# Kernel tuning notes

Hardware: AMD Instinct MI355X
Metric: run time of the kernel (lower is better)

## Reference

```python
import jax, jax.numpy as jnp
import numpy as np

N_NODES = 100000
N_EDGES = 1000000
D = 128          # in_features
C = 86           # out_classes (DDI relation types)


def setup_inputs() -> dict:
    key = jax.random.key(0)
    k_h, k_src, k_dst, k_w1, k_b1, k_w2, k_b2 = jax.random.split(key, 7)
    h = jax.random.normal(k_h, (N_NODES, D), dtype=jnp.float32)
    src = jax.random.randint(k_src, (N_EDGES,), 0, N_NODES, dtype=jnp.int64)
    dst = jax.random.randint(k_dst, (N_EDGES,), 0, N_NODES, dtype=jnp.int64)
    # nn.Linear default init: U(-1/sqrt(fan_in), 1/sqrt(fan_in))
    lim1 = 1.0 / np.sqrt(2 * D)
    W1 = jax.random.uniform(k_w1, (2 * D, D), jnp.float32, -lim1, lim1)
    b1 = jax.random.uniform(k_b1, (D,), jnp.float32, -lim1, lim1)
    lim2 = 1.0 / np.sqrt(D)
    W2 = jax.random.uniform(k_w2, (D, C), jnp.float32, -lim2, lim2)
    b2 = jax.random.uniform(k_b2, (C,), jnp.float32, -lim2, lim2)
    return {"h": h, "W1": W1, "b1": b1, "W2": W2, "b2": b2,
            "src": src, "dst": dst}


def reference(h, W1, b1, W2, b2, src, dst):
    # Gather per-edge src/dst node features: [E, D] each
    h_u = h[src]
    h_v = h[dst]
    # Split W1 along its input dim instead of materializing concat [E, 2D]
    # (same math as cat([h_u, h_v], 1) @ W1)
    W1u, W1v = W1[:D], W1[D:]
    hid = jax.nn.relu(h_u @ W1u + h_v @ W1v + b1)   # [E, D]
    score = hid @ W2 + b2                            # [E, C]
    return score
```

## Files before the change

kernel.cpp:

```cpp
#include <hip/hip_runtime.h>


typedef short bf16x8 __attribute__((ext_vector_type(8)));
typedef float f32x4 __attribute__((ext_vector_type(4)));

#define DIM 128
#define C_OUT 86
#define NPAD 96
#define HSTRIDE 136

__device__ __forceinline__ float bf2f(unsigned short u) {
    unsigned int x = ((unsigned int)u) << 16;
    float f;
    __builtin_memcpy(&f, &x, 4);
    return f;
}
__device__ __forceinline__ unsigned short f2bf(float f) {
    unsigned int x;
    __builtin_memcpy(&x, &f, 4);
    x = x + 0x7fffu + ((x >> 16) & 1u);
    return (unsigned short)(x >> 16);
}

__global__ __launch_bounds__(256) void node_gemm_kernel(
    const float* __restrict__ h, const float* __restrict__ W1,
    unsigned short* __restrict__ PQ, int n_nodes)
{
    __shared__ float As[64][33];
    __shared__ float Bs[32][64];
    const int t = threadIdx.x;
    const int m0 = blockIdx.x * 64;
    const int n0 = blockIdx.y * 64;
    const float* Bbase = (n0 < 128) ? (W1 + n0) : (W1 + 128 * 128 + (n0 - 128));
    const int tx = t & 15, ty = t >> 4;
    float acc[4][4] = {};
    for (int k0 = 0; k0 < 128; k0 += 32) {
#pragma unroll
        for (int i = 0; i < 2; ++i) {
            int f = t + i * 256;
            int r = f >> 3;
            int kc = (f & 7) << 2;
            int gr = m0 + r;
            float4 v = make_float4(0.f, 0.f, 0.f, 0.f);
            if (gr < n_nodes) v = *(const float4*)(h + (size_t)gr * DIM + k0 + kc);
            As[r][kc + 0] = v.x; As[r][kc + 1] = v.y;
            As[r][kc + 2] = v.z; As[r][kc + 3] = v.w;
        }
#pragma unroll
        for (int i = 0; i < 2; ++i) {
            int f = t + i * 256;
            int kk = f >> 4;
            int jc = (f & 15) << 2;
            *(float4*)&Bs[kk][jc] = *(const float4*)(Bbase + (size_t)(k0 + kk) * DIM + jc);
        }
        __syncthreads();
#pragma unroll
        for (int kk = 0; kk < 32; ++kk) {
            float a[4], b[4];
#pragma unroll
            for (int r = 0; r < 4; ++r) a[r] = As[ty * 4 + r][kk];
#pragma unroll
            for (int c = 0; c < 4; ++c) b[c] = Bs[kk][tx * 4 + c];
#pragma unroll
            for (int r = 0; r < 4; ++r)
#pragma unroll
                for (int c = 0; c < 4; ++c) acc[r][c] += a[r] * b[c];
        }
        __syncthreads();
    }
#pragma unroll
    for (int r = 0; r < 4; ++r) {
        int gm = m0 + ty * 4 + r;
        if (gm < n_nodes) {
            ushort4 o = make_ushort4(f2bf(acc[r][0]), f2bf(acc[r][1]),
                                     f2bf(acc[r][2]), f2bf(acc[r][3]));
            *(ushort4*)(PQ + (size_t)gm * 256 + n0 + tx * 4) = o;
        }
    }
}

__global__ __launch_bounds__(256) void edge_mlp_kernel(
    const unsigned short* __restrict__ PQ,
    const float* __restrict__ b1,
    const float* __restrict__ W2,
    const float* __restrict__ b2,
    const int* __restrict__ src,
    const int* __restrict__ dst,
    float* __restrict__ out,
    int n_edges)
{
    __shared__ unsigned short W2T[NPAD * HSTRIDE];
    __shared__ unsigned short hidL[64 * HSTRIDE];
    __shared__ float b1s[DIM];
    __shared__ float b2s[NPAD];

    const int t = threadIdx.x;
    for (int i = t; i < NPAD * DIM; i += 256) {
        int n = i >> 7;
        int k = i & 127;
        float v = (n < C_OUT) ? W2[(size_t)k * C_OUT + n] : 0.f;
        W2T[n * HSTRIDE + k] = f2bf(v);
    }
    if (t < DIM) b1s[t] = b1[t];
    if (t < NPAD) b2s[t] = (t < C_OUT) ? b2[t] : 0.f;
    __syncthreads();

    const int lane = t & 63;
    const int wv = t >> 6;
    const int m = lane & 15;
    const int quad = lane >> 4;

    bf16x8 Bfrag[6][4];
#pragma unroll
    for (int nt = 0; nt < 6; ++nt)
#pragma unroll
        for (int kt = 0; kt < 4; ++kt)
            Bfrag[nt][kt] = *(const bf16x8*)&W2T[(nt * 16 + m) * HSTRIDE + kt * 32 + quad * 8];

    const ushort4* PQ4 = (const ushort4*)PQ;

    for (int e0 = blockIdx.x * 64; e0 < n_edges; e0 += gridDim.x * 64) {
#pragma unroll
        for (int i = 0; i < 8; ++i) {
            int qi = t + i * 256;
            int e = qi >> 5;
            int q = qi & 31;
            int edge = e0 + e;
            ushort4 hv = make_ushort4(0, 0, 0, 0);
            if (edge < n_edges) {
                int s = src[edge];
                int d = dst[edge];
                ushort4 pv = PQ4[(size_t)s * 64 + q];
                ushort4 qv = PQ4[(size_t)d * 64 + 32 + q];
                int k = q << 2;
                float4 bb = *(const float4*)&b1s[k];
                float x0 = fmaxf(bf2f(pv.x) + bf2f(qv.x) + bb.x, 0.f);
                float x1 = fmaxf(bf2f(pv.y) + bf2f(qv.y) + bb.y, 0.f);
                float x2 = fmaxf(bf2f(pv.z) + bf2f(qv.z) + bb.z, 0.f);
                float x3 = fmaxf(bf2f(pv.w) + bf2f(qv.w) + bb.w, 0.f);
                hv = make_ushort4(f2bf(x0), f2bf(x1), f2bf(x2), f2bf(x3));
            }
            *(ushort4*)&hidL[e * HSTRIDE + (q << 2)] = hv;
        }
        __syncthreads();

        bf16x8 af[4];
#pragma unroll
        for (int kt = 0; kt < 4; ++kt)
            af[kt] = *(const bf16x8*)&hidL[(wv * 16 + m) * HSTRIDE + kt * 32 + quad * 8];

#pragma unroll
        for (int nt = 0; nt < 6; ++nt) {
            f32x4 acc = {0.f, 0.f, 0.f, 0.f};
#pragma unroll
            for (int kt = 0; kt < 4; ++kt)
                acc = __builtin_amdgcn_mfma_f32_16x16x32_bf16(af[kt], Bfrag[nt][kt], acc, 0, 0, 0);
            int col = nt * 16 + m;
            if (col < C_OUT) {
                float bias = b2s[col];
                int ebase = e0 + wv * 16 + quad * 4;
#pragma unroll
                for (int r = 0; r < 4; ++r) {
                    int edge = ebase + r;
                    if (edge < n_edges)
                        out[(size_t)edge * C_OUT + col] = acc[r] + bias;
                }
            }
        }
        __syncthreads();
    }
}

extern "C" void kernel_launch(void* const* d_in, const int* in_sizes, int n_in,
                              void* d_out, int out_size, void* d_ws, size_t ws_size,
                              hipStream_t stream) {
    const float* h  = (const float*)d_in[0];
    const float* W1 = (const float*)d_in[1];
    const float* b1 = (const float*)d_in[2];
    const float* W2 = (const float*)d_in[3];
    const float* b2 = (const float*)d_in[4];
    const int* src  = (const int*)d_in[5];
    const int* dst  = (const int*)d_in[6];
    float* out = (float*)d_out;
    const int n_nodes = in_sizes[0] / DIM;
    const int n_edges = in_sizes[5];
    unsigned short* PQ = (unsigned short*)d_ws;

    node_gemm_kernel<<<dim3((n_nodes + 63) / 64, 4), 256, 0, stream>>>(h, W1, PQ, n_nodes);
    edge_mlp_kernel<<<dim3(768), 256, 0, stream>>>(PQ, b1, W2, b2, src, dst, out, n_edges);
}
```

Before: 620.7 us.

## Use MFMA with split-bf16 for node GEMM and gather edge rows directly into registers

The node GEMM moves from scalar fp32 FMAs to bf16 MFMA. Each h value is split into a high and a low bf16 part to keep accuracy close to fp32, W1 is pre-packed in LDS in fragment layout, and b1 is folded into the Q half. The edge kernel drops the shared-memory hidden staging and its barriers: each lane gathers its edge's P and Q rows as 16-byte vectors straight into MFMA A fragments. W2 fragments are read from LDS instead of being held in registers, and both kernels get persistent grids and occupancy hints. In exchange the node GEMM does twice the MFMA work and writes scalar bf16 stores, and bf16 rounding of PQ and the hidden values remains.

New measurement: 865.8 us. 39.5% more time.

```diff
diff --git a/kernel.cpp b/kernel.cpp
--- a/kernel.cpp
+++ b/kernel.cpp
@@ -7,7 +7,6 @@
 #define DIM 128
 #define C_OUT 86
 #define NPAD 96
-#define HSTRIDE 136
 
 __device__ __forceinline__ float bf2f(unsigned short u) {
     unsigned int x = ((unsigned int)u) << 16;
@@ -22,66 +21,75 @@
     return (unsigned short)(x >> 16);
 }
 
-__global__ __launch_bounds__(256) void node_gemm_kernel(
+__global__ __launch_bounds__(256, 5) void node_gemm_kernel(
     const float* __restrict__ h, const float* __restrict__ W1,
+    const float* __restrict__ b1,
     unsigned short* __restrict__ PQ, int n_nodes)
 {
-    __shared__ float As[64][33];
-    __shared__ float Bs[32][64];
+    __shared__ unsigned short W1p[8 * 4 * 64 * 8];
     const int t = threadIdx.x;
-    const int m0 = blockIdx.x * 64;
-    const int n0 = blockIdx.y * 64;
-    const float* Bbase = (n0 < 128) ? (W1 + n0) : (W1 + 128 * 128 + (n0 - 128));
-    const int tx = t & 15, ty = t >> 4;
-    float acc[4][4] = {};
-    for (int k0 = 0; k0 < 128; k0 += 32) {
+    const int half = blockIdx.y;
+
+    for (int i = t; i < 128 * 128; i += 256) {
+        int k = i >> 7;
+        int jn = i & 127;
+        float v = W1[(size_t)(half * 128 + k) * 128 + jn];
+        int nt = jn >> 4, m = jn & 15;
+        int kt = k >> 5, quad = (k >> 3) & 3, jj = k & 7;
+        W1p[(((nt * 4 + kt) * 64) + quad * 16 + m) * 8 + jj] = f2bf(v);
+    }
+    __syncthreads();
+
+    const int lane = t & 63;
+    const int wv = t >> 6;
+    const int m = lane & 15;
+    const int quad = lane >> 4;
+    const bf16x8* bp = (const bf16x8*)W1p;
+
+    float bias[8];
 #pragma unroll
-        for (int i = 0; i < 2; ++i) {
-            int f = t + i * 256;
-            int r = f >> 3;
-            int kc = (f & 7) << 2;
-            int gr = m0 + r;
-            float4 v = make_float4(0.f, 0.f, 0.f, 0.f);
-            if (gr < n_nodes) v = *(const float4*)(h + (size_t)gr * DIM + k0 + kc);
-            As[r][kc + 0] = v.x; As[r][kc + 1] = v.y;
-            As[r][kc + 2] = v.z; As[r][kc + 3] = v.w;
+    for (int nt = 0; nt < 8; ++nt) bias[nt] = half ? b1[nt * 16 + m] : 0.f;
+
+    for (int m0 = blockIdx.x * 64; m0 < n_nodes; m0 += gridDim.x * 64) {
+        int row = m0 + wv * 16 + m;
+        int rowc = row < n_nodes ? row : n_nodes - 1;
+        const float* hrow = h + (size_t)rowc * DIM;
+        bf16x8 ahi[4], alo[4];
+#pragma unroll
+        for (int kt = 0; kt < 4; ++kt) {
+            float4 a0 = *(const float4*)(hrow + kt * 32 + quad * 8);
+            float4 a1 = *(const float4*)(hrow + kt * 32 + quad * 8 + 4);
+            float a[8] = {a0.x, a0.y, a0.z, a0.w, a1.x, a1.y, a1.z, a1.w};
+#pragma unroll
+            for (int j = 0; j < 8; ++j) {
+                unsigned short hb = f2bf(a[j]);
+                ahi[kt][j] = (short)hb;
+                alo[kt][j] = (short)f2bf(a[j] - bf2f(hb));
+            }
         }
 #pragma unroll
-        for (int i = 0; i < 2; ++i) {
-            int f = t + i * 256;
-            int kk = f >> 4;
-            int jc = (f & 15) << 2;
-            *(float4*)&Bs[kk][jc] = *(const float4*)(Bbase + (size_t)(k0 + kk) * DIM + jc);
-        }
-        __syncthreads();
+        for (int nt = 0; nt < 8; ++nt) {
+            f32x4 acc = {0.f, 0.f, 0.f, 0.f};
 #pragma unroll
-        for (int kk = 0; kk < 32; ++kk) {
-            float a[4], b[4];
+            for (int kt = 0; kt < 4; ++kt) {
+                bf16x8 bf = bp[(nt * 4 + kt) * 64 + lane];
+                acc = __builtin_amdgcn_mfma_f32_16x16x32_bf16(ahi[kt], bf, acc, 0, 0, 0);
+                acc = __builtin_amdgcn_mfma_f32_16x16x32_bf16(alo[kt], bf, acc, 0, 0, 0);
+            }
+            int rbase = m0 + wv * 16 + quad * 4;
+            int col = half * 128 + nt * 16 + m;
 #pragma unroll
-            for (int r = 0; r < 4; ++r) a[r] = As[ty * 4 + r][kk];
-#pragma unroll
-            for (int c = 0; c < 4; ++c) b[c] = Bs[kk][tx * 4 + c];
-#pragma unroll
-            for (int r = 0; r < 4; ++r)
-#pragma unroll
-                for (int c = 0; c < 4; ++c) acc[r][c] += a[r] * b[c];
-        }
-        __syncthreads();
-    }
-#pragma unroll
-    for (int r = 0; r < 4; ++r) {
-        int gm = m0 + ty * 4 + r;
-        if (gm < n_nodes) {
-            ushort4 o = make_ushort4(f2bf(acc[r][0]), f2bf(acc[r][1]),
-                                     f2bf(acc[r][2]), f2bf(acc[r][3]));
-            *(ushort4*)(PQ + (size_t)gm * 256 + n0 + tx * 4) = o;
+            for (int r = 0; r < 4; ++r) {
+                int ro = rbase + r;
+                if (ro < n_nodes)
+                    PQ[(size_t)ro * 256 + col] = f2bf(acc[r] + bias[nt]);
+            }
         }
     }
 }
 
-__global__ __launch_bounds__(256) void edge_mlp_kernel(
+__global__ __launch_bounds__(256, 6) void edge_mlp_kernel(
     const unsigned short* __restrict__ PQ,
-    const float* __restrict__ b1,
     const float* __restrict__ W2,
     const float* __restrict__ b2,
     const int* __restrict__ src,
@@ -89,85 +97,74 @@
     float* __restrict__ out,
     int n_edges)
 {
-    __shared__ unsigned short W2T[NPAD * HSTRIDE];
-    __shared__ unsigned short hidL[64 * HSTRIDE];
-    __shared__ float b1s[DIM];
-    __shared__ float b2s[NPAD];
+    __shared__ unsigned short W2p[6 * 4 * 64 * 8];
+    const int t = threadIdx.x;
 
-    const int t = threadIdx.x;
-    for (int i = t; i < NPAD * DIM; i += 256) {
-        int n = i >> 7;
-        int k = i & 127;
-        float v = (n < C_OUT) ? W2[(size_t)k * C_OUT + n] : 0.f;
-        W2T[n * HSTRIDE + k] = f2bf(v);
+    for (int i = t; i < 128 * 128; i += 256) {
+        int k = i >> 7;
+        int n = i & 127;
+        if (n < NPAD) {
+            float v = (n < C_OUT) ? W2[(size_t)k * C_OUT + n] : 0.f;
+            int nt = n >> 4, mm = n & 15;
+            int kt = k >> 5, qq = (k >> 3) & 3, jj = k & 7;
+            W2p[(((nt * 4 + kt) * 64) + qq * 16 + mm) * 8 + jj] = f2bf(v);
+        }
     }
-    if (t < DIM) b1s[t] = b1[t];
-    if (t < NPAD) b2s[t] = (t < C_OUT) ? b2[t] : 0.f;
     __syncthreads();
 
     const int lane = t & 63;
     const int wv = t >> 6;
     const int m = lane & 15;
     const int quad = lane >> 4;
+    const bf16x8* bp = (const bf16x8*)W2p;
 
-    bf16x8 Bfrag[6][4];
+    float bias[6];
 #pragma unroll
-    for (int nt = 0; nt < 6; ++nt)
-#pragma unroll
-        for (int kt = 0; kt < 4; ++kt)
-            Bfrag[nt][kt] = *(const bf16x8*)&W2T[(nt * 16 + m) * HSTRIDE + kt * 32 + quad * 8];
+    for (int nt = 0; nt < 6; ++nt) {
+        int col = nt * 16 + m;
+        bias[nt] = (col < C_OUT) ? b2[col] : 0.f;
+    }
 
-    const ushort4* PQ4 = (const ushort4*)PQ;
-
-    for (int e0 = blockIdx.x * 64; e0 < n_edges; e0 += gridDim.x * 64) {
-#pragma unroll
-        for (int i = 0; i < 8; ++i) {
-            int qi = t + i * 256;
-            int e = qi >> 5;
-            int q = qi & 31;
-            int edge = e0 + e;
-            ushort4 hv = make_ushort4(0, 0, 0, 0);
-            if (edge < n_edges) {
-                int s = src[edge];
-                int d = dst[edge];
-                ushort4 pv = PQ4[(size_t)s * 64 + q];
-                ushort4 qv = PQ4[(size_t)d * 64 + 32 + q];
-                int k = q << 2;
-                float4 bb = *(const float4*)&b1s[k];
-                float x0 = fmaxf(bf2f(pv.x) + bf2f(qv.x) + bb.x, 0.f);
-                float x1 = fmaxf(bf2f(pv.y) + bf2f(qv.y) + bb.y, 0.f);
-                float x2 = fmaxf(bf2f(pv.z) + bf2f(qv.z) + bb.z, 0.f);
-                float x3 = fmaxf(bf2f(pv.w) + bf2f(qv.w) + bb.w, 0.f);
-                hv = make_ushort4(f2bf(x0), f2bf(x1), f2bf(x2), f2bf(x3));
-            }
-            *(ushort4*)&hidL[e * HSTRIDE + (q << 2)] = hv;
-        }
-        __syncthreads();
+    const int last = n_edges - 1;
+    for (int c = blockIdx.x; c * 64 < n_edges; c += gridDim.x) {
+        const int e0 = c * 64;
+        int e = e0 + wv * 16 + m;
+        int ec = e <= last ? e : last;
+        int s = src[ec];
+        int d = dst[ec];
+        const bf16x8* Pp = (const bf16x8*)(PQ + (size_t)s * 256);
+        const bf16x8* Qp = (const bf16x8*)(PQ + (size_t)d * 256 + 128);
 
         bf16x8 af[4];
 #pragma unroll
-        for (int kt = 0; kt < 4; ++kt)
-            af[kt] = *(const bf16x8*)&hidL[(wv * 16 + m) * HSTRIDE + kt * 32 + quad * 8];
+        for (int kt = 0; kt < 4; ++kt) {
+            bf16x8 p = Pp[kt * 4 + quad];
+            bf16x8 q = Qp[kt * 4 + quad];
+#pragma unroll
+            for (int j = 0; j < 8; ++j) {
+                float x = bf2f((unsigned short)p[j]) + bf2f((unsigned short)q[j]);
+                af[kt][j] = (short)f2bf(fmaxf(x, 0.f));
+            }
+        }
 
 #pragma unroll
         for (int nt = 0; nt < 6; ++nt) {
             f32x4 acc = {0.f, 0.f, 0.f, 0.f};
 #pragma unroll
             for (int kt = 0; kt < 4; ++kt)
-                acc = __builtin_amdgcn_mfma_f32_16x16x32_bf16(af[kt], Bfrag[nt][kt], acc, 0, 0, 0);
+                acc = __builtin_amdgcn_mfma_f32_16x16x32_bf16(af[kt], bp[(nt * 4 + kt) * 64 + lane], acc, 0, 0, 0);
             int col = nt * 16 + m;
             if (col < C_OUT) {
-                float bias = b2s[col];
+                float bb = bias[nt];
                 int ebase = e0 + wv * 16 + quad * 4;
 #pragma unroll
                 for (int r = 0; r < 4; ++r) {
-                    int edge = ebase + r;
-                    if (edge < n_edges)
-                        out[(size_t)edge * C_OUT + col] = acc[r] + bias;
+                    int eo = ebase + r;
+                    if (eo < n_edges)
+                        out[(size_t)eo * C_OUT + col] = acc[r] + bb;
                 }
             }
         }
-        __syncthreads();
     }
 }
 
@@ -186,6 +183,6 @@
     const int n_edges = in_sizes[5];
     unsigned short* PQ = (unsigned short*)d_ws;
 
-    node_gemm_kernel<<<dim3((n_nodes + 63) / 64, 4), 256, 0, stream>>>(h, W1, PQ, n_nodes);
-    edge_mlp_kernel<<<dim3(768), 256, 0, stream>>>(PQ, b1, W2, b2, src, dst, out, n_edges);
+    node_gemm_kernel<<<dim3(512, 2), 256, 0, stream>>>(h, W1, b1, PQ, n_nodes);
+    edge_mlp_kernel<<<dim3(2048), 256, 0, stream>>>(PQ, W2, b2, src, dst, out, n_edges);
 }
```
